# Kernel tuning notes

Hardware: AMD Instinct MI355X
Metric: run time of the kernel (lower is better)

Reference implementation:

```python
import jax, jax.numpy as jnp
import numpy as np
from jax import lax

# ---- hyperparameters from opt ----
CONV_SIZE = 5          # box-blur kernel size
SQRT_FRAGS = 8         # h/sqrt_frags = patch size (non-overlapping unfold)
TH1_INIT = 0.5         # initial threshold (carried across fragments, as in torch)
PATCH_MEAN = 0.1       # target fraction of on-pixels per fragment
MORPH = 5              # morphology (max/min pool) window, stride 1, pad MORPH//2
TOL = 0.02
STEP = 0.0005

H = W = 4096


def setup_inputs() -> dict:
    key = jax.random.key(0)
    x = jax.random.uniform(key, (1, 1, H, W), dtype=jnp.float32)  # image in [0,1]
    blur_k = jnp.full((1, 1, CONV_SIZE, CONV_SIZE), 1.0 / CONV_SIZE ** 2,
                      dtype=jnp.float32)  # box filter, matches torch.full(...)
    return {"x": x, "blur_k": blur_k}


def _threshold_patches(patches):
    """Sequential per-fragment threshold bisection, th carried across fragments
    exactly like the torch loop mutating self.th1."""
    def frac(patch, t):  # mean of where(patch > t, 1, 0)
        return jnp.mean((patch > t).astype(jnp.float32))

    def frag_step(th, patch):
        # while mean(threshed) < target + 0.02: th -= 0.0005
        th = lax.while_loop(lambda t: frac(patch, t) < PATCH_MEAN + TOL,
                            lambda t: t - STEP, th)
        # while mean(threshed) > target - 0.02: th += 0.0005
        th = lax.while_loop(lambda t: frac(patch, t) > PATCH_MEAN - TOL,
                            lambda t: t + STEP, th)
        return th, (patch > th).astype(jnp.float32)

    _, threshed = lax.scan(frag_step, jnp.float32(TH1_INIT), patches)
    return threshed  # [SF^2, k, k]


def _morph_pool(x, is_max):
    pad = MORPH // 2
    op = x if is_max else -x
    r = lax.reduce_window(op, -jnp.inf, lax.max,
                          (1, 1, MORPH, MORPH), (1, 1, 1, 1),
                          [(0, 0), (0, 0), (pad, pad), (pad, pad)])
    return r if is_max else -r


def reference(x, blur_k):
    N, c, h, w = x.shape  # N = c = 1
    k = h // SQRT_FRAGS
    # box blur, padding='same'
    conved = lax.conv_general_dilated(x.reshape(-1, 1, h, w), blur_k,
                                      (1, 1), "SAME").reshape(N, c, h, w)
    # F.unfold with kernel=stride=k -> non-overlapping patches, row-major order
    patches = (conved.reshape(SQRT_FRAGS, k, SQRT_FRAGS, k)
               .transpose(0, 2, 1, 3)
               .reshape(SQRT_FRAGS ** 2, k, k))
    threshed = lax.stop_gradient(_threshold_patches(patches))
    # F.fold: inverse of the unfold above
    folded = (threshed.reshape(SQRT_FRAGS, SQRT_FRAGS, k, k)
              .transpose(0, 2, 1, 3)
              .reshape(N, c, h, w))
    # morphological close: max-pool then min-pool (min_pool = -maxpool(-x))
    out = _morph_pool(_morph_pool(folded, True), False)
    return out
```

## Files before the change

kernel.cpp:

```cpp
#include <hip/hip_runtime.h>
#include <stdint.h>

#define HH 4096
#define WW 4096
#define NPIX (HH * WW)
#define NBINS 8192
#define NFRAG 64
#define FRAG_PIX (512 * 512)
#define WPR 64
#define NWORDS (HH * WPR)
#define CAP 4096
#define LCAP 2048

#define RANK_HI 230686u
#define RANK_LO 241172u

typedef unsigned long long u64;

__device__ __forceinline__ int frag_of(int py, int px) {
  return ((py >> 9) << 3) + (px >> 9);
}

__device__ __forceinline__ int bin_of(float v) {
  int b = (int)(v * 8192.0f);
  if (b < 0) b = 0;
  if (b > NBINS - 1) b = NBINS - 1;
  return b;
}

__device__ __forceinline__ u64 spread4(u64 x) {
  x &= 0xFFFFull;
  x = (x | (x << 24)) & 0x000000FF000000FFull;
  x = (x | (x << 12)) & 0x000F000F000F000Full;
  x = (x | (x << 6))  & 0x0303030303030303ull;
  x = (x | (x << 3))  & 0x1111111111111111ull;
  return x;
}

__device__ __forceinline__ float blur_tree(const float rowbuf[5][8], int e) {
  const float K = (float)(1.0 / 25.0);
  float p[25];
#pragma unroll
  for (int i = 0; i < 25; ++i) {
    p[i] = __fmul_rn(rowbuf[i / 5][e + (i % 5)], K);
  }
  float r0 = __fadd_rn(__fadd_rn(p[0], p[8]),  p[16]);
  float r1 = __fadd_rn(__fadd_rn(p[1], p[9]),  p[17]);
  float r2 = __fadd_rn(__fadd_rn(p[2], p[10]), p[18]);
  float r3 = __fadd_rn(__fadd_rn(p[3], p[11]), p[19]);
  float r4 = __fadd_rn(__fadd_rn(p[4], p[12]), p[20]);
  float r5 = __fadd_rn(__fadd_rn(p[5], p[13]), p[21]);
  float r6 = __fadd_rn(__fadd_rn(p[6], p[14]), p[22]);
  float r7 = __fadd_rn(__fadd_rn(p[7], p[15]), p[23]);
  float res = __fadd_rn(
      __fadd_rn(__fadd_rn(r0, r1), __fadd_rn(r2, r3)),
      __fadd_rn(__fadd_rn(r4, r5), __fadd_rn(r6, r7)));
  return __fadd_rn(res, p[24]);
}

__global__ void __launch_bounds__(512)
blur_hist_kernel(const float* __restrict__ x,
                 float* __restrict__ out,
                 uint32_t* __restrict__ hist) {
  __shared__ uint32_t lh[NBINS];
  int tid = threadIdx.x;
  for (int i = tid; i < NBINS; i += 512) lh[i] = 0;
  __syncthreads();
  int f = blockIdx.x >> 4;
  int s = blockIdx.x & 15;
  int row0 = (f >> 3) * 512 + s * 32;
  int col0 = (f & 7) * 512;
  for (int it = tid; it < 8 * 128; it += 512) {
    int pr = it >> 7;
    int c4 = it & 127;
    int py = row0 + pr * 4;
    int px = col0 + c4 * 4;
    float rb[8][8];
    bool interior = (px >= 2) && (px + 5 < WW);
#pragma unroll
    for (int r = 0; r < 8; ++r) {
      int yy = py - 2 + r;
      if ((unsigned)yy >= (unsigned)HH) {
#pragma unroll
        for (int j = 0; j < 8; ++j) rb[r][j] = 0.0f;
      } else if (interior) {
        const float* rp = x + (size_t)yy * WW + px;
        float2 L = *(const float2*)(rp - 2);
        float4 M = *(const float4*)(rp);
        float2 R = *(const float2*)(rp + 4);
        rb[r][0] = L.x; rb[r][1] = L.y;
        rb[r][2] = M.x; rb[r][3] = M.y;
        rb[r][4] = M.z; rb[r][5] = M.w;
        rb[r][6] = R.x; rb[r][7] = R.y;
      } else {
#pragma unroll
        for (int j = 0; j < 8; ++j) {
          int xx = px - 2 + j;
          rb[r][j] = ((unsigned)xx < (unsigned)WW) ? x[(size_t)yy * WW + xx] : 0.0f;
        }
      }
    }
#pragma unroll
    for (int orow = 0; orow < 4; ++orow) {
      float4 res;
      res.x = blur_tree(rb + orow, 0);
      res.y = blur_tree(rb + orow, 1);
      res.z = blur_tree(rb + orow, 2);
      res.w = blur_tree(rb + orow, 3);
      *(float4*)(out + (size_t)(py + orow) * WW + px) = res;
      atomicAdd(&lh[bin_of(res.x)], 1u);
      atomicAdd(&lh[bin_of(res.y)], 1u);
      atomicAdd(&lh[bin_of(res.z)], 1u);
      atomicAdd(&lh[bin_of(res.w)], 1u);
    }
  }
  __syncthreads();
  uint32_t* hf = hist + f * NBINS;
  int start = ((s << 9) + tid) & (NBINS - 1);
  for (int ii = 0; ii < NBINS; ii += 512) {
    int i = (start + ii) & (NBINS - 1);
    uint32_t c = lh[i];
    if (c) atomicAdd(&hf[i], c);
  }
}

__global__ void findcrit_kernel(const uint32_t* __restrict__ hist,
                                int4* __restrict__ bins4) {
  __shared__ uint32_t segsum[256];
  __shared__ uint32_t segoff[256];
  __shared__ int4 result;
  int f = blockIdx.x;
  int tid = threadIdx.x;
  const uint32_t* hf = hist + f * NBINS;
  int base = tid * 32;
  uint32_t h32[32];
  uint32_t s = 0;
  for (int i = 0; i < 32; ++i) { h32[i] = hf[base + i]; s += h32[i]; }
  segsum[tid] = s;
  __syncthreads();
  if (tid == 0) {
    uint32_t a = 0;
    for (int i = 0; i < 256; ++i) { segoff[i] = a; a += segsum[i]; }
  }
  __syncthreads();
  uint32_t st = segoff[tid];
  uint32_t en = st + segsum[tid];
  if (st <= RANK_HI && RANK_HI < en) {
    uint32_t a = st;
    for (int i = 0; i < 32; ++i) {
      uint32_t nx = a + h32[i];
      if (RANK_HI < nx) { result.x = base + i; result.z = (int)(RANK_HI - a); break; }
      a = nx;
    }
  }
  if (st <= RANK_LO && RANK_LO < en) {
    uint32_t a = st;
    for (int i = 0; i < 32; ++i) {
      uint32_t nx = a + h32[i];
      if (RANK_LO < nx) { result.y = base + i; result.w = (int)(RANK_LO - a); break; }
      a = nx;
    }
  }
  __syncthreads();
  if (tid == 0) bins4[f] = result;
}

__global__ void __launch_bounds__(256)
gather_kernel(const float* __restrict__ blur,
              const int4* __restrict__ bins4,
              float* __restrict__ band,
              uint32_t* __restrict__ bandcnt) {
  __shared__ float lval[LCAP];
  __shared__ uint32_t lcnt;
  __shared__ uint32_t gbase;
  int f = blockIdx.x >> 4;
  int s = blockIdx.x & 15;
  int tid = threadIdx.x;
  if (tid == 0) lcnt = 0;
  __syncthreads();
  int row0 = (f >> 3) * 512 + s * 32;
  int col0 = (f & 7) * 512;
  int4 info = bins4[f];
  for (int it = tid; it < 32 * 128; it += 256) {
    int rr = it >> 7, c4 = it & 127;
    float4 v = *(const float4*)(blur + (size_t)(row0 + rr) * WW + col0 + c4 * 4);
    float vv[4] = {v.x, v.y, v.z, v.w};
#pragma unroll
    for (int e = 0; e < 4; ++e) {
      int b = bin_of(vv[e]);
      if (b == info.x || b == info.y) {
        uint32_t p = atomicAdd(&lcnt, 1u);
        if (p < LCAP) lval[p] = vv[e];
        else {
          uint32_t pos = atomicAdd(&bandcnt[f], 1u);
          if (pos < CAP) band[(size_t)f * CAP + pos] = vv[e];
        }
      }
    }
  }
  __syncthreads();
  uint32_t n = lcnt < LCAP ? lcnt : LCAP;
  if (tid == 0) gbase = atomicAdd(&bandcnt[f], n);
  __syncthreads();
  uint32_t base = gbase;
  for (uint32_t i = tid; i < n; i += 256) {
    uint32_t pos = base + i;
    if (pos < CAP) band[(size_t)f * CAP + pos] = lval[i];
  }
}

__global__ void select_kernel(const float* __restrict__ band,
                              const uint32_t* __restrict__ bandcnt,
                              const int4* __restrict__ bins4,
                              float2* __restrict__ vhl) {
  __shared__ float wv[CAP];
  __shared__ float res[2];
  int f = blockIdx.x;
  int tid = threadIdx.x;
  int n = (int)bandcnt[f];
  if (n > CAP) n = CAP;
  for (int i = tid; i < n; i += 256) wv[i] = band[(size_t)f * CAP + i];
  __syncthreads();
  int4 info = bins4[f];
#pragma unroll
  for (int sel = 0; sel < 2; ++sel) {
    int tb = sel ? info.y : info.x;
    int k  = sel ? info.w : info.z;
    for (int i = tid; i < n; i += 256) {
      float w = wv[i];
      if (bin_of(w) != tb) continue;
      int less = 0, leq = 0;
      for (int j = 0; j < n; ++j) {
        float u = wv[j];
        if (bin_of(u) == tb) {
          less += (u < w) ? 1 : 0;
          leq  += (u <= w) ? 1 : 0;
        }
      }
      if (less <= k && k < leq) res[sel] = w;
    }
  }
  __syncthreads();
  if (tid == 0) vhl[f] = make_float2(res[0], res[1]);
}

__global__ void walk_kernel(const float2* __restrict__ vhl, float* __restrict__ th_out) {
  int lane = threadIdx.x;
  float2 mine = vhl[lane];
  float th = 0.5f;
  for (int f = 0; f < NFRAG; ++f) {
    float VH = __shfl(mine.x, f);
    float VL = __shfl(mine.y, f);
    while (th >= VH) {
#pragma unroll
      for (int i = 0; i < 16; ++i) {
        float t2 = __fadd_rn(th, -0.0005f);
        th = (th >= VH) ? t2 : th;
      }
    }
    while (th < VL) {
#pragma unroll
      for (int i = 0; i < 16; ++i) {
        float t2 = __fadd_rn(th, 0.0005f);
        th = (th < VL) ? t2 : th;
      }
    }
    if (lane == 0) th_out[f] = th;
  }
}

__global__ void __launch_bounds__(256)
mask_pack_kernel(const float* __restrict__ blur,
                 const float* __restrict__ th,
                 u64* __restrict__ pk) {
  const int T = NPIX / 16;
  int t = blockIdx.x * blockDim.x + threadIdx.x;
  float4 v[4];
#pragma unroll
  for (int k = 0; k < 4; ++k) {
    v[k] = *(const float4*)(blur + (size_t)(t + k * T) * 4);
  }
  int lane = threadIdx.x & 63;
#pragma unroll
  for (int k = 0; k < 4; ++k) {
    int g = t + k * T;
    int p0 = g * 4;
    float tf = th[frag_of(p0 >> 12, p0 & (WW - 1))];
    u64 b0 = __ballot(v[k].x > tf);
    u64 b1 = __ballot(v[k].y > tf);
    u64 b2 = __ballot(v[k].z > tf);
    u64 b3 = __ballot(v[k].w > tf);
    if ((lane & 15) == 0) {
      int sh = lane;
      u64 w = spread4(b0 >> sh) | (spread4(b1 >> sh) << 1)
            | (spread4(b2 >> sh) << 2) | (spread4(b3 >> sh) << 3);
      int base_word = ((g - lane) * 4) >> 6;
      pk[base_word + (lane >> 4)] = w;
    }
  }
}

__global__ void dilate_kernel(const u64* __restrict__ in, u64* __restrict__ out) {
  __shared__ u64 hm[68][16];
  int bx = blockIdx.x & 3;
  int by = blockIdx.x >> 2;
  int r0 = by * 64, c0 = bx * 16;
  int tid = threadIdx.x;
  for (int it = tid; it < 68 * 16; it += 256) {
    int rr = it >> 4;
    int cc = it & 15;
    int gy = r0 - 2 + rr;
    int gx = c0 + cc;
    u64 m = 0, l = 0, r = 0;
    if ((unsigned)gy < (unsigned)HH) {
      m = in[gy * WPR + gx];
      l = (gx > 0) ? in[gy * WPR + gx - 1] : 0ull;
      r = (gx < WPR - 1) ? in[gy * WPR + gx + 1] : 0ull;
    }
    hm[rr][cc] = m | (m << 1) | (m << 2) | (m >> 1) | (m >> 2)
                   | (l >> 62) | (l >> 63) | (r << 62) | (r << 63);
  }
  __syncthreads();
  for (int it = tid; it < 64 * 16; it += 256) {
    int rr = it >> 4;
    int cc = it & 15;
    u64 v = hm[rr][cc] | hm[rr + 1][cc] | hm[rr + 2][cc] | hm[rr + 3][cc] | hm[rr + 4][cc];
    out[(r0 + rr) * WPR + c0 + cc] = v;
  }
}

__global__ void erode_unpack_kernel(const u64* __restrict__ in, float* __restrict__ out) {
  __shared__ u64 hm[68][16];
  __shared__ u64 d2[64][16];
  int bx = blockIdx.x & 3;
  int by = blockIdx.x >> 2;
  int r0 = by * 64, c0 = bx * 16;
  int tid = threadIdx.x;
  for (int it = tid; it < 68 * 16; it += 256) {
    int rr = it >> 4;
    int cc = it & 15;
    int gy = r0 - 2 + rr;
    int gx = c0 + cc;
    u64 m = 0, l = 0, r = 0;
    if ((unsigned)gy < (unsigned)HH) {
      m = ~in[gy * WPR + gx];
      l = (gx > 0) ? ~in[gy * WPR + gx - 1] : 0ull;
      r = (gx < WPR - 1) ? ~in[gy * WPR + gx + 1] : 0ull;
    }
    hm[rr][cc] = m | (m << 1) | (m << 2) | (m >> 1) | (m >> 2)
                   | (l >> 62) | (l >> 63) | (r << 62) | (r << 63);
  }
  __syncthreads();
  for (int it = tid; it < 64 * 16; it += 256) {
    int rr = it >> 4;
    int cc = it & 15;
    d2[rr][cc] = hm[rr][cc] | hm[rr + 1][cc] | hm[rr + 2][cc] | hm[rr + 3][cc] | hm[rr + 4][cc];
  }
  __syncthreads();
  int colbase = c0 * 64;
  for (int it = tid; it < 64 * 256; it += 256) {
    int rr = it >> 8;
    int px0 = (it & 255) * 4;
    u64 w = d2[rr][px0 >> 6];
    int sh = px0 & 63;
    float4 o;
    o.x = (float)(1 - (int)((w >> (sh + 0)) & 1ull));
    o.y = (float)(1 - (int)((w >> (sh + 1)) & 1ull));
    o.z = (float)(1 - (int)((w >> (sh + 2)) & 1ull));
    o.w = (float)(1 - (int)((w >> (sh + 3)) & 1ull));
    *(float4*)(out + (size_t)(r0 + rr) * WW + colbase + px0) = o;
  }
}

extern "C" void kernel_launch(void* const* d_in, const int* in_sizes, int n_in,
                              void* d_out, int out_size, void* d_ws, size_t ws_size,
                              hipStream_t stream) {
  const float* x = (const float*)d_in[0];
  if (n_in > 1 && in_sizes[0] != NPIX) x = (const float*)d_in[1];
  float* out = (float*)d_out;
  char* ws = (char*)d_ws;

  const size_t OFF_HIST = 0;
  const size_t OFF_BCNT = 2097152;
  const size_t OFF_TH   = 2097408;
  const size_t OFF_PKA  = 2097664;
  const size_t OFF_PKB  = 4194816;
  const size_t OFF_BINS = 6291968;
  const size_t OFF_VHL  = 6292992;
  const size_t OFF_BAND = 6293504;
  const size_t OFF_BLUR = 8388608;
  const size_t WS_NEED  = OFF_BLUR + (size_t)NPIX * sizeof(float);
  uint32_t* hist    = (uint32_t*)(ws + OFF_HIST);
  uint32_t* bandcnt = (uint32_t*)(ws + OFF_BCNT);
  float*    th      = (float*)(ws + OFF_TH);
  u64*      PKA     = (u64*)(ws + OFF_PKA);
  u64*      PKB     = (u64*)(ws + OFF_PKB);
  int4*     bins4   = (int4*)(ws + OFF_BINS);
  float2*   vhl     = (float2*)(ws + OFF_VHL);
  float*    band    = (float*)(ws + OFF_BAND);

  float* blurred = (ws_size >= WS_NEED) ? (float*)(ws + OFF_BLUR) : out;

  const int TPB = 256;
  const int NB16 = NPIX / 16 / TPB;

  hipMemsetAsync(hist, 0, (size_t)NFRAG * NBINS * sizeof(uint32_t) + NFRAG * sizeof(uint32_t), stream);
  blur_hist_kernel<<<1024, 512, 0, stream>>>(x, blurred, hist);
  findcrit_kernel<<<NFRAG, TPB, 0, stream>>>(hist, bins4);
  gather_kernel<<<1024, TPB, 0, stream>>>(blurred, bins4, band, bandcnt);
  select_kernel<<<NFRAG, TPB, 0, stream>>>(band, bandcnt, bins4, vhl);
  walk_kernel<<<1, 64, 0, stream>>>(vhl, th);
  mask_pack_kernel<<<NB16, TPB, 0, stream>>>(blurred, th, PKA);
  dilate_kernel<<<256, TPB, 0, stream>>>(PKA, PKB);
  erode_unpack_kernel<<<256, TPB, 0, stream>>>(PKB, out);
}
```

Baseline: 260.2 us.

## Fuse dilate and erode into one morphology kernel and retile mask packing

Merges the separate dilate and erode+unpack kernels into one morph_kernel. It recomputes a haloed dilation tile in shared memory, so the intermediate packed bitmap no longer goes through global memory and one launch is saved. The tiles shrink to 16 rows by 16 words with a 2-word column halo, and the grid grows to 1024 blocks. Mask packing now gives each block a slice of a single fragment, so the threshold is loaded once per block instead of per element. The cost is some redundant halo loads and recomputation, plus more syncthreads stages per block.

```diff
diff --git a/kernel.cpp b/kernel.cpp
--- a/kernel.cpp
+++ b/kernel.cpp
@@ -273,23 +273,21 @@
 mask_pack_kernel(const float* __restrict__ blur,
                  const float* __restrict__ th,
                  u64* __restrict__ pk) {
-  const int T = NPIX / 16;
-  int t = blockIdx.x * blockDim.x + threadIdx.x;
-  float4 v[4];
-#pragma unroll
-  for (int k = 0; k < 4; ++k) {
-    v[k] = *(const float4*)(blur + (size_t)(t + k * T) * 4);
-  }
-  int lane = threadIdx.x & 63;
-#pragma unroll
-  for (int k = 0; k < 4; ++k) {
-    int g = t + k * T;
-    int p0 = g * 4;
-    float tf = th[frag_of(p0 >> 12, p0 & (WW - 1))];
-    u64 b0 = __ballot(v[k].x > tf);
-    u64 b1 = __ballot(v[k].y > tf);
-    u64 b2 = __ballot(v[k].z > tf);
-    u64 b3 = __ballot(v[k].w > tf);
+  int f = blockIdx.x >> 4;
+  int s = blockIdx.x & 15;
+  int tid = threadIdx.x;
+  int lane = tid & 63;
+  int row0 = (f >> 3) * 512 + s * 32;
+  int col0 = (f & 7) * 512;
+  float tf = th[f];
+  for (int it = tid; it < 32 * 128; it += 256) {
+    int rr = it >> 7, c4 = it & 127;
+    float4 v = *(const float4*)(blur + (size_t)(row0 + rr) * WW + col0 + c4 * 4);
+    int g = ((row0 + rr) << 10) + (col0 >> 2) + c4;
+    u64 b0 = __ballot(v.x > tf);
+    u64 b1 = __ballot(v.y > tf);
+    u64 b2 = __ballot(v.z > tf);
+    u64 b3 = __ballot(v.w > tf);
     if ((lane & 15) == 0) {
       int sh = lane;
       u64 w = spread4(b0 >> sh) | (spread4(b1 >> sh) << 1)
@@ -300,75 +298,60 @@
   }
 }
 
-__global__ void dilate_kernel(const u64* __restrict__ in, u64* __restrict__ out) {
-  __shared__ u64 hm[68][16];
+__global__ void __launch_bounds__(256)
+morph_kernel(const u64* __restrict__ in, float* __restrict__ out) {
+  __shared__ u64 pkin[24][20];
+  __shared__ u64 hA[24][20];
+  __shared__ u64 nD[20][20];
+  __shared__ u64 hB[20][20];
   int bx = blockIdx.x & 3;
   int by = blockIdx.x >> 2;
-  int r0 = by * 64, c0 = bx * 16;
-  int tid = threadIdx.x;
-  for (int it = tid; it < 68 * 16; it += 256) {
-    int rr = it >> 4;
-    int cc = it & 15;
-    int gy = r0 - 2 + rr;
-    int gx = c0 + cc;
-    u64 m = 0, l = 0, r = 0;
-    if ((unsigned)gy < (unsigned)HH) {
+  int R0 = by * 16, W0 = bx * 16;
+  int tid = threadIdx.x;
+  for (int it = tid; it < 24 * 20; it += 256) {
+    int i = it / 20, j = it % 20;
+    int gy = R0 - 4 + i, gx = W0 - 2 + j;
+    u64 m = 0;
+    if ((unsigned)gy < (unsigned)HH && (unsigned)gx < (unsigned)WPR)
       m = in[gy * WPR + gx];
-      l = (gx > 0) ? in[gy * WPR + gx - 1] : 0ull;
-      r = (gx < WPR - 1) ? in[gy * WPR + gx + 1] : 0ull;
-    }
-    hm[rr][cc] = m | (m << 1) | (m << 2) | (m >> 1) | (m >> 2)
-                   | (l >> 62) | (l >> 63) | (r << 62) | (r << 63);
-  }
-  __syncthreads();
-  for (int it = tid; it < 64 * 16; it += 256) {
-    int rr = it >> 4;
-    int cc = it & 15;
-    u64 v = hm[rr][cc] | hm[rr + 1][cc] | hm[rr + 2][cc] | hm[rr + 3][cc] | hm[rr + 4][cc];
-    out[(r0 + rr) * WPR + c0 + cc] = v;
-  }
-}
-
-__global__ void erode_unpack_kernel(const u64* __restrict__ in, float* __restrict__ out) {
-  __shared__ u64 hm[68][16];
-  __shared__ u64 d2[64][16];
-  int bx = blockIdx.x & 3;
-  int by = blockIdx.x >> 2;
-  int r0 = by * 64, c0 = bx * 16;
-  int tid = threadIdx.x;
-  for (int it = tid; it < 68 * 16; it += 256) {
-    int rr = it >> 4;
-    int cc = it & 15;
-    int gy = r0 - 2 + rr;
-    int gx = c0 + cc;
-    u64 m = 0, l = 0, r = 0;
-    if ((unsigned)gy < (unsigned)HH) {
-      m = ~in[gy * WPR + gx];
-      l = (gx > 0) ? ~in[gy * WPR + gx - 1] : 0ull;
-      r = (gx < WPR - 1) ? ~in[gy * WPR + gx + 1] : 0ull;
-    }
-    hm[rr][cc] = m | (m << 1) | (m << 2) | (m >> 1) | (m >> 2)
-                   | (l >> 62) | (l >> 63) | (r << 62) | (r << 63);
-  }
-  __syncthreads();
-  for (int it = tid; it < 64 * 16; it += 256) {
-    int rr = it >> 4;
-    int cc = it & 15;
-    d2[rr][cc] = hm[rr][cc] | hm[rr + 1][cc] | hm[rr + 2][cc] | hm[rr + 3][cc] | hm[rr + 4][cc];
-  }
-  __syncthreads();
-  int colbase = c0 * 64;
-  for (int it = tid; it < 64 * 256; it += 256) {
-    int rr = it >> 8;
+    pkin[i][j] = m;
+  }
+  __syncthreads();
+  for (int it = tid; it < 24 * 18; it += 256) {
+    int i = it / 18, j = 1 + it % 18;
+    u64 m = pkin[i][j], l = pkin[i][j - 1], r = pkin[i][j + 1];
+    hA[i][j] = m | (m << 1) | (m << 2) | (m >> 1) | (m >> 2)
+                 | (l >> 62) | (l >> 63) | (r << 62) | (r << 63);
+  }
+  __syncthreads();
+  for (int it = tid; it < 20 * 18; it += 256) {
+    int i = it / 18, j = 1 + it % 18;
+    u64 v = hA[i][j] | hA[i + 1][j] | hA[i + 2][j] | hA[i + 3][j] | hA[i + 4][j];
+    int gy = R0 - 2 + i, gx = W0 - 2 + j;
+    nD[i][j] = ((unsigned)gy < (unsigned)HH && (unsigned)gx < (unsigned)WPR)
+                   ? ~v : 0ull;
+  }
+  __syncthreads();
+  for (int it = tid; it < 20 * 16; it += 256) {
+    int i = it / 16, j = 2 + it % 16;
+    u64 m = nD[i][j], l = nD[i][j - 1], r = nD[i][j + 1];
+    hB[i][j] = m | (m << 1) | (m << 2) | (m >> 1) | (m >> 2)
+                 | (l >> 62) | (l >> 63) | (r << 62) | (r << 63);
+  }
+  __syncthreads();
+  int colbase = W0 * 64;
+  for (int it = tid; it < 16 * 256; it += 256) {
+    int o = it >> 8;
     int px0 = (it & 255) * 4;
-    u64 w = d2[rr][px0 >> 6];
+    int j = 2 + (px0 >> 6);
+    u64 v = hB[o][j] | hB[o + 1][j] | hB[o + 2][j] | hB[o + 3][j] | hB[o + 4][j];
     int sh = px0 & 63;
-    float4 o;
-    o.x = (float)(1 - (int)((w >> (sh + 0)) & 1ull));
-    o.y = (float)(1 - (int)((w >> (sh + 1)) & 1ull));
-    o.z = (float)(1 - (int)((w >> (sh + 2)) & 1ull));
-    o.w = (float)(1 - (int)((w >> (sh + 3)) & 1ull));
-    *(float4*)(out + (size_t)(r0 + rr) * WW + colbase + px0) = o;
+    float4 ov;
+    ov.x = (float)(1 - (int)((v >> (sh + 0)) & 1ull));
+    ov.y = (float)(1 - (int)((v >> (sh + 1)) & 1ull));
+    ov.z = (float)(1 - (int)((v >> (sh + 2)) & 1ull));
+    ov.w = (float)(1 - (int)((v >> (sh + 3)) & 1ull));
+    *(float4*)(out + (size_t)(R0 + o) * WW + colbase + px0) = ov;
   }
 }
 
@@ -394,15 +377,14 @@
   uint32_t* bandcnt = (uint32_t*)(ws + OFF_BCNT);
   float*    th      = (float*)(ws + OFF_TH);
   u64*      PKA     = (u64*)(ws + OFF_PKA);
-  u64*      PKB     = (u64*)(ws + OFF_PKB);
   int4*     bins4   = (int4*)(ws + OFF_BINS);
   float2*   vhl     = (float2*)(ws + OFF_VHL);
   float*    band    = (float*)(ws + OFF_BAND);
+  (void)OFF_PKB;
 
   float* blurred = (ws_size >= WS_NEED) ? (float*)(ws + OFF_BLUR) : out;
 
   const int TPB = 256;
-  const int NB16 = NPIX / 16 / TPB;
 
   hipMemsetAsync(hist, 0, (size_t)NFRAG * NBINS * sizeof(uint32_t) + NFRAG * sizeof(uint32_t), stream);
   blur_hist_kernel<<<1024, 512, 0, stream>>>(x, blurred, hist);
@@ -410,7 +392,6 @@
   gather_kernel<<<1024, TPB, 0, stream>>>(blurred, bins4, band, bandcnt);
   select_kernel<<<NFRAG, TPB, 0, stream>>>(band, bandcnt, bins4, vhl);
   walk_kernel<<<1, 64, 0, stream>>>(vhl, th);
-  mask_pack_kernel<<<NB16, TPB, 0, stream>>>(blurred, th, PKA);
-  dilate_kernel<<<256, TPB, 0, stream>>>(PKA, PKB);
-  erode_unpack_kernel<<<256, TPB, 0, stream>>>(PKB, out);
-}
+  mask_pack_kernel<<<1024, TPB, 0, stream>>>(blurred, th, PKA);
+  morph_kernel<<<1024, TPB, 0, stream>>>(PKA, out);
+}
```

Result: faster. 253.9 us (-2.4%).
